# Kernel tuning notes

Measured on AMD Instinct MI355X. Metric: run time of the kernel, lower is better.

Reference implementation:

```python
import jax, jax.numpy as jnp
import numpy as np

K = 3          # kernel_size
STRIDE = 1
PAD = 1
NCAPS = 32     # num_capsules
CCH = 16       # caps_channels
NIT = 3        # num_iterations


def extract_patches(x, k, stride, pad):
    # x: [B, C, H, W] -> [B, oh, ow, k, k, C]  (Tile2d + permute in the original)
    xp = jnp.pad(x, ((0, 0), (0, 0), (pad, pad), (pad, pad)))
    B, C, H, W = xp.shape
    oh = (H - k) // stride + 1
    ow = (W - k) // stride + 1
    tiles = [xp[:, :, i:i + stride * (oh - 1) + 1:stride, j:j + stride * (ow - 1) + 1:stride]
             for i in range(k) for j in range(k)]  # fixed k*k loop, not a data-dim loop
    p = jnp.stack(tiles, 0).reshape(k, k, B, C, oh, ow)
    return p.transpose(2, 4, 5, 0, 1, 3)


def setup_inputs() -> dict:
    key = jax.random.key(0)
    k1, k2 = jax.random.split(key)
    input = jax.random.normal(k1, (8, 128, 32, 32), dtype=jnp.float32)
    weight = jax.random.normal(k2, (1, 1, 1, K, K, 128, NCAPS * CCH), dtype=jnp.float32)
    bias = jnp.zeros((1, 1, 1, K, K, 1, NCAPS * CCH), dtype=jnp.float32)
    return {"input": input, "weight": weight, "bias": bias}


def reference(input, weight, bias):
    chunks = extract_patches(input, K, STRIDE, PAD)            # [B,oh,ow,k,k,C]
    C = weight.shape[-2]
    NC = weight.shape[-1]
    w = weight.reshape(K, K, C, NC)
    b = bias.reshape(K, K, NC)
    # priors = (patch vectors) @ W + bias : [B,oh,ow,k,k,NC]
    priors = jnp.einsum('bhwijc,ijcn->bhwijn', chunks, w) + b
    B, oh, ow = priors.shape[:3]
    priors = priors.reshape(B, oh, ow, K * K, NCAPS, CCH)
    outputs = priors.mean(3, keepdims=True)                    # [B,oh,ow,1,NCAPS,CCH]
    for _ in range(NIT):
        d = outputs - priors
        # cluster_weight: 1/sqrt(||d||^2 + 1e-4)
        cw = 1.0 / jnp.sqrt(jnp.sum(d * d, axis=-1, keepdims=True) + 1e-4)
        cw = cw / jnp.sum(cw, axis=3, keepdims=True)
        outputs = jnp.sum(priors * cw, axis=3, keepdims=True)
    out = outputs.reshape(B, oh, ow, NCAPS * CCH)
    return jnp.transpose(out, (0, 3, 1, 2))                    # [B, NCAPS*CCH, oh, ow]
```

## Files before the change

### kernel.cpp

```cpp
#include <hip/hip_runtime.h>


typedef __bf16 bf16x8 __attribute__((ext_vector_type(8)));
typedef float  f32x4  __attribute__((ext_vector_type(4)));

#define NC    512
#define CIN   128
#define HW    32
#define INT_H 34
#define INT_W 34
#define ROWB  (INT_W * 256)
#define WT_ELEMS (9 * NC * CIN)

__global__ __launch_bounds__(256)
void prepass(const float* __restrict__ in, const float* __restrict__ wgt,
             __bf16* __restrict__ wT, __bf16* __restrict__ inT) {
    const int t = threadIdx.x;
    if (blockIdx.x < 288) {
        int g   = blockIdx.x * 256 + t;
        int n   = g & 511;
        int cb  = (g >> 9) & 15;
        int tap = g >> 13;
        bf16x8 v;
        #pragma unroll
        for (int k = 0; k < 8; k++)
            v[k] = (__bf16)wgt[(tap * CIN + cb * 8 + k) * NC + n];
        *(bf16x8*)(wT + ((size_t)tap * NC + n) * CIN + cb * 8) = v;
    } else {
        int g    = (blockIdx.x - 288) * 256 + t;
        int cb   = g & 15;
        int cell = g >> 4;
        int w    = cell % INT_W;
        int rest = cell / INT_W;
        int h    = rest % INT_H;
        int b    = rest / INT_H;
        bf16x8 v;
        #pragma unroll
        for (int k = 0; k < 8; k++) v[k] = (__bf16)0.0f;
        if (h >= 1 && h <= 32 && w >= 1 && w <= 32) {
            #pragma unroll
            for (int k = 0; k < 8; k++)
                v[k] = (__bf16)in[((b * CIN + cb * 8 + k) * HW + (h - 1)) * HW + (w - 1)];
        }
        int within = (cb * 16) ^ ((w & 15) << 4);
        *(bf16x8*)((char*)inT + (size_t)(b * INT_H + h) * ROWB + w * 256 + within) = v;
    }
}

__global__ __launch_bounds__(256, 2)
void caps_main(const __bf16* __restrict__ wT, const __bf16* __restrict__ inT,
               const float* __restrict__ bias, float* __restrict__ out) {
    __shared__ __attribute__((aligned(16))) unsigned char ring[4 * ROWB];

    const int x    = blockIdx.x;
    const int nblk = x & 7;
    const int hg   = (x >> 3) & 7;
    const int b    = x >> 6;
    const int h0   = hg * 4;
    const int t    = threadIdx.x;
    const int lane = t & 63;
    const int wm   = t >> 6;
    const int l15  = lane & 15;
    const int l4   = lane >> 4;
    const int nb   = nblk * 64 + wm * 16;

    const char* ibase = (const char*)inT + (size_t)(b * INT_H) * ROWB;

    auto stage_row = [&](int row, int slot) {
        const char* src = ibase + (size_t)row * ROWB;
        unsigned char* dst = ring + slot * ROWB;
        int c = wm * 2;
        __builtin_amdgcn_global_load_lds((const unsigned*)(src + c * 1024 + lane * 16),
                                         (unsigned*)(dst + c * 1024), 16, 0, 0);
        __builtin_amdgcn_global_load_lds((const unsigned*)(src + (c + 1) * 1024 + lane * 16),
                                         (unsigned*)(dst + (c + 1) * 1024), 16, 0, 0);
        if (wm == 3 && lane < 32)
            __builtin_amdgcn_global_load_lds((const unsigned*)(src + 8192 + lane * 16),
                                             (unsigned*)(dst + 8192), 16, 0, 0);
    };

    bf16x8 afrag[9][4];
    {
        const __bf16* aptr = wT + (size_t)(nb + l15) * CIN + l4 * 8;
        #pragma unroll
        for (int tap = 0; tap < 9; tap++)
            #pragma unroll
            for (int kk = 0; kk < 4; kk++)
                afrag[tap][kk] = *(const bf16x8*)(aptr + (size_t)(tap * NC) * CIN + kk * 32);
    }

    stage_row(h0 + 0, 0);
    stage_row(h0 + 1, 1);
    stage_row(h0 + 2, 2);

    for (int r = 0; r < 4; ++r) {
        __syncthreads();
        if (r < 3) stage_row(h0 + r + 3, (r + 3) & 3);

        #pragma unroll 1
        for (int nf = 0; nf < 2; ++nf) {
            f32x4 acc[9];
            #pragma unroll
            for (int tap = 0; tap < 9; tap++)
                acc[tap] = *(const f32x4*)(bias + tap * NC + nb + l4 * 4);

            #pragma unroll
            for (int i = 0; i < 3; i++) {
                const unsigned char* rowp = ring + ((r + i) & 3) * ROWB;
                #pragma unroll
                for (int j = 0; j < 3; j++) {
                    const int tap = i * 3 + j;
                    #pragma unroll
                    for (int kk = 0; kk < 4; kk++) {
                        int pos = j + nf * 16 + l15;
                        int off = pos * 256 + ((kk * 64 + l4 * 16) ^ ((pos & 15) << 4));
                        bf16x8 bv = *(const bf16x8*)(rowp + off);
                        acc[tap] =
                            __builtin_amdgcn_mfma_f32_16x16x32_bf16(afrag[tap][kk], bv,
                                                                    acc[tap], 0, 0, 0);
                    }
                }
            }

            f32x4 o = acc[0];
            #pragma unroll
            for (int tap = 1; tap < 9; tap++) o += acc[tap];
            o = o * (1.0f / 9.0f);

            #pragma unroll
            for (int it = 0; it < 3; it++) {
                float cw[9];
                float S = 0.f;
                #pragma unroll
                for (int tap = 0; tap < 9; tap++) {
                    f32x4 d = o - acc[tap];
                    float d2 = d[0] * d[0] + d[1] * d[1] + d[2] * d[2] + d[3] * d[3];
                    d2 += __shfl_xor(d2, 16);
                    d2 += __shfl_xor(d2, 32);
                    float rr = __builtin_amdgcn_rsqf(d2 + 1e-4f);
                    cw[tap] = rr;
                    S += rr;
                }
                float inv = __builtin_amdgcn_rcpf(S);
                f32x4 on = acc[0] * cw[0];
                #pragma unroll
                for (int tap = 1; tap < 9; tap++) on += acc[tap] * cw[tap];
                o = on * inv;
            }

            const int hr = h0 + r;
            size_t obase = ((size_t)(b * NC + nb + l4 * 4) * HW + hr) * HW + nf * 16 + l15;
            #pragma unroll
            for (int reg = 0; reg < 4; reg++)
                out[obase + (size_t)reg * HW * HW] = o[reg];
        }
    }
}

extern "C" void kernel_launch(void* const* d_in, const int* in_sizes, int n_in,
                              void* d_out, int out_size, void* d_ws, size_t ws_size,
                              hipStream_t stream) {
    const float* in   = (const float*)d_in[0];
    const float* wgt  = (const float*)d_in[1];
    const float* bias = (const float*)d_in[2];
    float* out = (float*)d_out;

    __bf16* wT  = (__bf16*)d_ws;
    __bf16* inT = wT + WT_ELEMS;

    prepass<<<866, 256, 0, stream>>>(in, wgt, wT, inT);

    caps_main<<<512, 256, 0, stream>>>(wT, inT, bias, out);
}
```

Measured before the change: 59.97 us.

## Switch to 32x32x16 MFMA with weights streamed from global, tile rows per block

Replaces the 16x16x32 MFMA path, which kept all nine tap weight fragments in registers, with 32x32x16 MFMAs. Weight fragments are now read from global/L2 per tap inside the loop instead of preloaded. Each block covers 128 capsule channels and two output rows instead of 64 channels and four rows, and loads all four needed input rows into LDS at once instead of a rolling ring. The routing reduction is split into two 8-element halves per lane with a single cross-lane shuffle. The larger MFMA tile is meant to raise compute density and cut register pressure from preloaded weights, at the cost of repeated weight loads and losing row-load/compute overlap.

```diff
diff --git a/kernel.cpp b/kernel.cpp
--- a/kernel.cpp
+++ b/kernel.cpp
@@ -3,6 +3,7 @@
 
 typedef __bf16 bf16x8 __attribute__((ext_vector_type(8)));
 typedef float  f32x4  __attribute__((ext_vector_type(4)));
+typedef float  f32x16 __attribute__((ext_vector_type(16)));
 
 #define NC    512
 #define CIN   128
@@ -50,109 +51,127 @@
 __global__ __launch_bounds__(256, 2)
 void caps_main(const __bf16* __restrict__ wT, const __bf16* __restrict__ inT,
                const float* __restrict__ bias, float* __restrict__ out) {
-    __shared__ __attribute__((aligned(16))) unsigned char ring[4 * ROWB];
+    __shared__ __attribute__((aligned(16))) unsigned char tile[4 * ROWB];
 
     const int x    = blockIdx.x;
-    const int nblk = x & 7;
-    const int hg   = (x >> 3) & 7;
+    const int nblk = x & 3;
+    const int hg   = (x >> 2) & 15;
     const int b    = x >> 6;
-    const int h0   = hg * 4;
+    const int h0   = hg * 2;
     const int t    = threadIdx.x;
     const int lane = t & 63;
     const int wm   = t >> 6;
-    const int l15  = lane & 15;
-    const int l4   = lane >> 4;
-    const int nb   = nblk * 64 + wm * 16;
+    const int l31  = lane & 31;
+    const int lk   = lane >> 5;
+    const int nb   = nblk * 128 + wm * 32;
 
-    const char* ibase = (const char*)inT + (size_t)(b * INT_H) * ROWB;
+    {
+        const char* ibase = (const char*)inT + (size_t)(b * INT_H + h0) * ROWB;
+        #pragma unroll
+        for (int row = 0; row < 4; row++) {
+            const char* src = ibase + (size_t)row * ROWB;
+            unsigned char* dst = tile + row * ROWB;
+            int c = wm * 2;
+            __builtin_amdgcn_global_load_lds((const unsigned*)(src + c * 1024 + lane * 16),
+                                             (unsigned*)(dst + c * 1024), 16, 0, 0);
+            __builtin_amdgcn_global_load_lds((const unsigned*)(src + (c + 1) * 1024 + lane * 16),
+                                             (unsigned*)(dst + (c + 1) * 1024), 16, 0, 0);
+            if (wm == 3 && lane < 32)
+                __builtin_amdgcn_global_load_lds((const unsigned*)(src + 8192 + lane * 16),
+                                                 (unsigned*)(dst + 8192), 16, 0, 0);
+        }
+    }
+    __syncthreads();
 
-    auto stage_row = [&](int row, int slot) {
-        const char* src = ibase + (size_t)row * ROWB;
-        unsigned char* dst = ring + slot * ROWB;
-        int c = wm * 2;
-        __builtin_amdgcn_global_load_lds((const unsigned*)(src + c * 1024 + lane * 16),
-                                         (unsigned*)(dst + c * 1024), 16, 0, 0);
-        __builtin_amdgcn_global_load_lds((const unsigned*)(src + (c + 1) * 1024 + lane * 16),
-                                         (unsigned*)(dst + (c + 1) * 1024), 16, 0, 0);
-        if (wm == 3 && lane < 32)
-            __builtin_amdgcn_global_load_lds((const unsigned*)(src + 8192 + lane * 16),
-                                             (unsigned*)(dst + 8192), 16, 0, 0);
-    };
+    #pragma unroll 1
+    for (int r = 0; r < 2; ++r) {
+        f32x16 acc[9];
+        #pragma unroll
+        for (int tap = 0; tap < 9; tap++) {
+            #pragma unroll
+            for (int q = 0; q < 4; q++) {
+                f32x4 bv = *(const f32x4*)(bias + tap * NC + nb + lk * 4 + q * 8);
+                acc[tap][q * 4 + 0] = bv[0];
+                acc[tap][q * 4 + 1] = bv[1];
+                acc[tap][q * 4 + 2] = bv[2];
+                acc[tap][q * 4 + 3] = bv[3];
+            }
+        }
 
-    bf16x8 afrag[9][4];
-    {
-        const __bf16* aptr = wT + (size_t)(nb + l15) * CIN + l4 * 8;
+        const int pos0 = l31;
         #pragma unroll
-        for (int tap = 0; tap < 9; tap++)
+        for (int i = 0; i < 3; i++) {
+            const unsigned char* rowp = tile + (r + i) * ROWB;
             #pragma unroll
-            for (int kk = 0; kk < 4; kk++)
-                afrag[tap][kk] = *(const bf16x8*)(aptr + (size_t)(tap * NC) * CIN + kk * 32);
-    }
-
-    stage_row(h0 + 0, 0);
-    stage_row(h0 + 1, 1);
-    stage_row(h0 + 2, 2);
-
-    for (int r = 0; r < 4; ++r) {
-        __syncthreads();
-        if (r < 3) stage_row(h0 + r + 3, (r + 3) & 3);
-
-        #pragma unroll 1
-        for (int nf = 0; nf < 2; ++nf) {
-            f32x4 acc[9];
-            #pragma unroll
-            for (int tap = 0; tap < 9; tap++)
-                acc[tap] = *(const f32x4*)(bias + tap * NC + nb + l4 * 4);
-
-            #pragma unroll
-            for (int i = 0; i < 3; i++) {
-                const unsigned char* rowp = ring + ((r + i) & 3) * ROWB;
+            for (int j = 0; j < 3; j++) {
+                const int tap = i * 3 + j;
+                const int pos = j + pos0;
+                const unsigned char* bp = rowp + pos * 256;
+                const int sw = (pos & 15) << 4;
+                const __bf16* ap = wT + (size_t)(tap * NC + nb + l31) * CIN + lk * 8;
                 #pragma unroll
-                for (int j = 0; j < 3; j++) {
-                    const int tap = i * 3 + j;
-                    #pragma unroll
-                    for (int kk = 0; kk < 4; kk++) {
-                        int pos = j + nf * 16 + l15;
-                        int off = pos * 256 + ((kk * 64 + l4 * 16) ^ ((pos & 15) << 4));
-                        bf16x8 bv = *(const bf16x8*)(rowp + off);
-                        acc[tap] =
-                            __builtin_amdgcn_mfma_f32_16x16x32_bf16(afrag[tap][kk], bv,
-                                                                    acc[tap], 0, 0, 0);
-                    }
+                for (int kk = 0; kk < 8; kk++) {
+                    bf16x8 a  = *(const bf16x8*)(ap + kk * 16);
+                    bf16x8 bv = *(const bf16x8*)(bp + (((kk * 32) + lk * 16) ^ sw));
+                    acc[tap] = __builtin_amdgcn_mfma_f32_32x32x16_bf16(a, bv, acc[tap], 0, 0, 0);
                 }
             }
+        }
 
-            f32x4 o = acc[0];
+        f32x16 o = acc[0];
+        #pragma unroll
+        for (int tap = 1; tap < 9; tap++) o += acc[tap];
+        o = o * (1.0f / 9.0f);
+
+        #pragma unroll
+        for (int it = 0; it < 3; it++) {
+            float cwa[9], cwb[9];
+            float Sa = 0.f, Sb = 0.f;
             #pragma unroll
-            for (int tap = 1; tap < 9; tap++) o += acc[tap];
-            o = o * (1.0f / 9.0f);
+            for (int tap = 0; tap < 9; tap++) {
+                float d2a = 0.f, d2b = 0.f;
+                #pragma unroll
+                for (int e = 0; e < 8; e++) {
+                    float d = o[e] - acc[tap][e];
+                    d2a = fmaf(d, d, d2a);
+                }
+                #pragma unroll
+                for (int e = 8; e < 16; e++) {
+                    float d = o[e] - acc[tap][e];
+                    d2b = fmaf(d, d, d2b);
+                }
+                d2a += __shfl_xor(d2a, 32);
+                d2b += __shfl_xor(d2b, 32);
+                float ra = __builtin_amdgcn_rsqf(d2a + 1e-4f);
+                float rb = __builtin_amdgcn_rsqf(d2b + 1e-4f);
+                cwa[tap] = ra;  Sa += ra;
+                cwb[tap] = rb;  Sb += rb;
+            }
+            float inva = __builtin_amdgcn_rcpf(Sa);
+            float invb = __builtin_amdgcn_rcpf(Sb);
+            f32x16 on;
+            #pragma unroll
+            for (int e = 0; e < 8; e++)  on[e] = acc[0][e] * cwa[0];
+            #pragma unroll
+            for (int e = 8; e < 16; e++) on[e] = acc[0][e] * cwb[0];
+            #pragma unroll
+            for (int tap = 1; tap < 9; tap++) {
+                #pragma unroll
+                for (int e = 0; e < 8; e++)  on[e] = fmaf(acc[tap][e], cwa[tap], on[e]);
+                #pragma unroll
+                for (int e = 8; e < 16; e++) on[e] = fmaf(acc[tap][e], cwb[tap], on[e]);
+            }
+            #pragma unroll
+            for (int e = 0; e < 8; e++)  o[e] = on[e] * inva;
+            #pragma unroll
+            for (int e = 8; e < 16; e++) o[e] = on[e] * invb;
+        }
 
-            #pragma unroll
-            for (int it = 0; it < 3; it++) {
-                float cw[9];
-                float S = 0.f;
-                #pragma unroll
-                for (int tap = 0; tap < 9; tap++) {
-                    f32x4 d = o - acc[tap];
-                    float d2 = d[0] * d[0] + d[1] * d[1] + d[2] * d[2] + d[3] * d[3];
-                    d2 += __shfl_xor(d2, 16);
-                    d2 += __shfl_xor(d2, 32);
-                    float rr = __builtin_amdgcn_rsqf(d2 + 1e-4f);
-                    cw[tap] = rr;
-                    S += rr;
-                }
-                float inv = __builtin_amdgcn_rcpf(S);
-                f32x4 on = acc[0] * cw[0];
-                #pragma unroll
-                for (int tap = 1; tap < 9; tap++) on += acc[tap] * cw[tap];
-                o = on * inv;
-            }
-
-            const int hr = h0 + r;
-            size_t obase = ((size_t)(b * NC + nb + l4 * 4) * HW + hr) * HW + nf * 16 + l15;
-            #pragma unroll
-            for (int reg = 0; reg < 4; reg++)
-                out[obase + (size_t)reg * HW * HW] = o[reg];
+        const int hr = h0 + r;
+        #pragma unroll
+        for (int reg = 0; reg < 16; reg++) {
+            int n = nb + (reg & 3) + 8 * (reg >> 2) + 4 * lk;
+            out[((size_t)(b * NC + n) * HW + hr) * HW + l31] = o[reg];
         }
     }
 }
```

Measured after the change: 140.9 us. +134.9%, slower.

## Split work to one output row per block and stream weights from global

Applied to the files above, without the earlier changes.

Each block now handles a single output row instead of four. Its three input rows are loaded into LDS once, with no ring buffer, and the grid grows from 512 to 2048 blocks. The register-resident weight fragments (36 bf16x8 per thread) are removed; weights are re-read from global/L2 inside the MFMA loop. This lowers register pressure so occupancy can rise to 4 blocks per SM and drops the row pipelining. The cost is more global weight traffic and more redundant input-row loads, since each row is now loaded by three blocks.

```diff
diff --git a/kernel.cpp b/kernel.cpp
--- a/kernel.cpp
+++ b/kernel.cpp
@@ -47,16 +47,16 @@
     }
 }
 
-__global__ __launch_bounds__(256, 2)
+__global__ __launch_bounds__(256, 4)
 void caps_main(const __bf16* __restrict__ wT, const __bf16* __restrict__ inT,
                const float* __restrict__ bias, float* __restrict__ out) {
-    __shared__ __attribute__((aligned(16))) unsigned char ring[4 * ROWB];
+    __shared__ __attribute__((aligned(16))) unsigned char brow[3 * ROWB];
 
     const int x    = blockIdx.x;
     const int nblk = x & 7;
-    const int hg   = (x >> 3) & 7;
-    const int b    = x >> 6;
-    const int h0   = hg * 4;
+    const int bh   = x >> 3;
+    const int h    = bh & 31;
+    const int b    = bh >> 5;
     const int t    = threadIdx.x;
     const int lane = t & 63;
     const int wm   = t >> 6;
@@ -64,96 +64,77 @@
     const int l4   = lane >> 4;
     const int nb   = nblk * 64 + wm * 16;
 
-    const char* ibase = (const char*)inT + (size_t)(b * INT_H) * ROWB;
+    {
+        const char* src = (const char*)inT + (size_t)(b * INT_H + h) * ROWB;
+        #pragma unroll
+        for (int i = 0; i < 7; i++) {
+            int c = wm + i * 4;
+            if (c < 25) {
+                __builtin_amdgcn_global_load_lds((const unsigned*)(src + c * 1024 + lane * 16),
+                                                 (unsigned*)(brow + c * 1024), 16, 0, 0);
+            } else if (c == 25 && lane < 32) {
+                __builtin_amdgcn_global_load_lds((const unsigned*)(src + c * 1024 + lane * 16),
+                                                 (unsigned*)(brow + c * 1024), 16, 0, 0);
+            }
+        }
+    }
+    __syncthreads();
 
-    auto stage_row = [&](int row, int slot) {
-        const char* src = ibase + (size_t)row * ROWB;
-        unsigned char* dst = ring + slot * ROWB;
-        int c = wm * 2;
-        __builtin_amdgcn_global_load_lds((const unsigned*)(src + c * 1024 + lane * 16),
-                                         (unsigned*)(dst + c * 1024), 16, 0, 0);
-        __builtin_amdgcn_global_load_lds((const unsigned*)(src + (c + 1) * 1024 + lane * 16),
-                                         (unsigned*)(dst + (c + 1) * 1024), 16, 0, 0);
-        if (wm == 3 && lane < 32)
-            __builtin_amdgcn_global_load_lds((const unsigned*)(src + 8192 + lane * 16),
-                                             (unsigned*)(dst + 8192), 16, 0, 0);
-    };
+    const __bf16* aptr = wT + (size_t)(nb + l15) * CIN + l4 * 8;
 
-    bf16x8 afrag[9][4];
-    {
-        const __bf16* aptr = wT + (size_t)(nb + l15) * CIN + l4 * 8;
+    #pragma unroll 1
+    for (int nf = 0; nf < 2; ++nf) {
+        f32x4 acc[9];
         #pragma unroll
         for (int tap = 0; tap < 9; tap++)
+            acc[tap] = *(const f32x4*)(bias + tap * NC + nb + l4 * 4);
+
+        #pragma unroll
+        for (int i = 0; i < 3; i++) {
             #pragma unroll
-            for (int kk = 0; kk < 4; kk++)
-                afrag[tap][kk] = *(const bf16x8*)(aptr + (size_t)(tap * NC) * CIN + kk * 32);
-    }
-
-    stage_row(h0 + 0, 0);
-    stage_row(h0 + 1, 1);
-    stage_row(h0 + 2, 2);
-
-    for (int r = 0; r < 4; ++r) {
-        __syncthreads();
-        if (r < 3) stage_row(h0 + r + 3, (r + 3) & 3);
-
-        #pragma unroll 1
-        for (int nf = 0; nf < 2; ++nf) {
-            f32x4 acc[9];
-            #pragma unroll
-            for (int tap = 0; tap < 9; tap++)
-                acc[tap] = *(const f32x4*)(bias + tap * NC + nb + l4 * 4);
-
-            #pragma unroll
-            for (int i = 0; i < 3; i++) {
-                const unsigned char* rowp = ring + ((r + i) & 3) * ROWB;
+            for (int j = 0; j < 3; j++) {
+                const int tap = i * 3 + j;
                 #pragma unroll
-                for (int j = 0; j < 3; j++) {
-                    const int tap = i * 3 + j;
-                    #pragma unroll
-                    for (int kk = 0; kk < 4; kk++) {
-                        int pos = j + nf * 16 + l15;
-                        int off = pos * 256 + ((kk * 64 + l4 * 16) ^ ((pos & 15) << 4));
-                        bf16x8 bv = *(const bf16x8*)(rowp + off);
-                        acc[tap] =
-                            __builtin_amdgcn_mfma_f32_16x16x32_bf16(afrag[tap][kk], bv,
-                                                                    acc[tap], 0, 0, 0);
-                    }
+                for (int kk = 0; kk < 4; kk++) {
+                    bf16x8 a = *(const bf16x8*)(aptr + (size_t)(tap * NC) * CIN + kk * 32);
+                    int pos = j + nf * 16 + l15;
+                    int off = i * ROWB + pos * 256 + ((kk * 64 + l4 * 16) ^ ((pos & 15) << 4));
+                    bf16x8 bv = *(const bf16x8*)(brow + off);
+                    acc[tap] = __builtin_amdgcn_mfma_f32_16x16x32_bf16(a, bv, acc[tap], 0, 0, 0);
                 }
             }
+        }
 
-            f32x4 o = acc[0];
+        f32x4 o = acc[0];
+        #pragma unroll
+        for (int tap = 1; tap < 9; tap++) o += acc[tap];
+        o = o * (1.0f / 9.0f);
+
+        #pragma unroll
+        for (int it = 0; it < 3; it++) {
+            float cw[9];
+            float S = 0.f;
             #pragma unroll
-            for (int tap = 1; tap < 9; tap++) o += acc[tap];
-            o = o * (1.0f / 9.0f);
+            for (int tap = 0; tap < 9; tap++) {
+                f32x4 d = o - acc[tap];
+                float d2 = d[0] * d[0] + d[1] * d[1] + d[2] * d[2] + d[3] * d[3];
+                d2 += __shfl_xor(d2, 16);
+                d2 += __shfl_xor(d2, 32);
+                float rr = __builtin_amdgcn_rsqf(d2 + 1e-4f);
+                cw[tap] = rr;
+                S += rr;
+            }
+            float inv = __builtin_amdgcn_rcpf(S);
+            f32x4 on = acc[0] * cw[0];
+            #pragma unroll
+            for (int tap = 1; tap < 9; tap++) on += acc[tap] * cw[tap];
+            o = on * inv;
+        }
 
-            #pragma unroll
-            for (int it = 0; it < 3; it++) {
-                float cw[9];
-                float S = 0.f;
-                #pragma unroll
-                for (int tap = 0; tap < 9; tap++) {
-                    f32x4 d = o - acc[tap];
-                    float d2 = d[0] * d[0] + d[1] * d[1] + d[2] * d[2] + d[3] * d[3];
-                    d2 += __shfl_xor(d2, 16);
-                    d2 += __shfl_xor(d2, 32);
-                    float rr = __builtin_amdgcn_rsqf(d2 + 1e-4f);
-                    cw[tap] = rr;
-                    S += rr;
-                }
-                float inv = __builtin_amdgcn_rcpf(S);
-                f32x4 on = acc[0] * cw[0];
-                #pragma unroll
-                for (int tap = 1; tap < 9; tap++) on += acc[tap] * cw[tap];
-                o = on * inv;
-            }
-
-            const int hr = h0 + r;
-            size_t obase = ((size_t)(b * NC + nb + l4 * 4) * HW + hr) * HW + nf * 16 + l15;
-            #pragma unroll
-            for (int reg = 0; reg < 4; reg++)
-                out[obase + (size_t)reg * HW * HW] = o[reg];
-        }
+        size_t obase = ((size_t)(b * NC + nb + l4 * 4) * HW + h) * HW + nf * 16 + l15;
+        #pragma unroll
+        for (int reg = 0; reg < 4; reg++)
+            out[obase + (size_t)reg * HW * HW] = o[reg];
     }
 }
 
@@ -170,5 +151,6 @@
 
     prepass<<<866, 256, 0, stream>>>(in, wgt, wT, inT);
 
-    caps_main<<<512, 256, 0, stream>>>(wT, inT, bias, out);
+    dim3 grid(256 * 8);
+    caps_main<<<grid, 256, 0, stream>>>(wT, inT, bias, out);
 }
```

Measured after the change: 152.4 us. +154.1%, slower.
